# Kernel tuning notes

Hardware: AMD Instinct MI355X
Metric: run time of the kernel (lower is better)

Reference implementation:

```python
import jax, jax.numpy as jnp
import numpy as np

B, T_Q, T_K, D = 16, 512, 1024, 512


def setup_inputs() -> dict:
    key = jax.random.key(0)
    k1, k2, k3, k4, k5 = jax.random.split(key, 5)
    query = jax.random.normal(k1, (B, T_Q, D), dtype=jnp.float32)
    keys = jax.random.normal(k2, (B, T_K, D), dtype=jnp.float32)
    # lengths in [T_K//2, T_K] so every query row has valid keys
    output_lengths = jax.random.randint(k3, (B,), T_K // 2, T_K + 1, dtype=jnp.int32)
    # linear_q params (PyTorch Linear: y = x @ W.T + b), kaiming-ish scale
    Wq = jax.random.normal(k4, (D, D), dtype=jnp.float32) * (1.0 / np.sqrt(D))
    bq = jax.random.normal(k5, (D,), dtype=jnp.float32) * 0.01
    scale = jnp.ones((1,), dtype=jnp.float32)
    return {"query": query, "keys": keys, "output_lengths": output_lengths,
            "Wq": Wq, "bq": bq, "scale": scale}


def reference(query, keys, output_lengths, Wq, bq, scale):
    # linear_q: b t_q d -> b t_q d
    att_query = jnp.einsum('bqe,de->bqd', query, Wq) + bq
    # dot_prod score with learned scalar scale: b t_q t_k
    scores = jnp.einsum('bqd,bkd->bqk', att_query, keys) * scale[0]
    # length mask over t_k (True = valid position)
    valid = jnp.arange(keys.shape[1]) < output_lengths[:, None]  # b t_k
    neg_inf = jnp.asarray(-jnp.inf, dtype=scores.dtype)
    scores = jnp.where(valid[:, None, :], scores, neg_inf)
    attn = jax.nn.softmax(scores, axis=2)  # dropout p=0 -> identity
    # context = attn @ values, values == keys
    context = jnp.einsum('bqk,bkd->bqd', attn, keys)
    return context, attn
```

## Files before the change

### kernel.cpp

```cpp
#include <hip/hip_runtime.h>
#include <math.h>

#define BB 16
#define TQ 512
#define TK 1024
#define DD 512

typedef __bf16 bf16x8 __attribute__((ext_vector_type(8)));
typedef __bf16 bf16x4v __attribute__((ext_vector_type(4)));
typedef _Float16 f16x8 __attribute__((ext_vector_type(8)));
typedef _Float16 f16x4v __attribute__((ext_vector_type(4)));
typedef float f32x4 __attribute__((ext_vector_type(4)));

template<int TM, bool SPLIT, bool BT, bool BIAS, bool SCALE>
__global__ __launch_bounds__(256) void mfma_gemm(
    const float* __restrict__ A, const float* __restrict__ Bm,
    float* __restrict__ C, const float* __restrict__ bias,
    const float* __restrict__ scl,
    int N, int K, long sA, long sB, long sC)
{
    constexpr int WI  = TM / 32;
    constexpr int LDT = 40;
    __shared__ unsigned short As_hi[TM * LDT];
    __shared__ unsigned short Bs_hi[128 * LDT];
    __shared__ unsigned short As_lo[SPLIT ? TM * LDT : 8];
    __shared__ unsigned short Bs_lo[SPLIT ? 128 * LDT : 8];

    const int bz = blockIdx.z;
    A  += (long)bz * sA;
    Bm += (long)bz * sB;
    C  += (long)bz * sC;

    const int m0 = blockIdx.y * TM;
    const int n0 = blockIdx.x * 128;
    const int tid  = threadIdx.x;
    const int lane = tid & 63;
    const int wave = tid >> 6;
    const int wm0 = (wave >> 1) * (TM / 2);
    const int wn0 = (wave & 1) * 64;
    const int fm = lane & 15;
    const int fq = lane >> 4;

    f32x4 acc[WI][4];
    #pragma unroll
    for (int i = 0; i < WI; ++i)
        #pragma unroll
        for (int j = 0; j < 4; ++j) {
            f32x4 z = {0.f, 0.f, 0.f, 0.f};
            acc[i][j] = z;
        }

    for (int k0 = 0; k0 < K; k0 += 32) {
        #pragma unroll
        for (int i = 0; i < WI; ++i) {
            const int s   = tid + i * 256;
            const int row = s >> 3;
            const int c4  = (s & 7) << 2;
            const float4 v = *(const float4*)(A + (long)(m0 + row) * K + k0 + c4);
            if (SPLIT) {
                const __bf16 h0 = (__bf16)v.x, h1 = (__bf16)v.y,
                             h2 = (__bf16)v.z, h3 = (__bf16)v.w;
                bf16x4v hv = {h0, h1, h2, h3};
                *(bf16x4v*)&As_hi[row * LDT + c4] = hv;
                bf16x4v lv = {(__bf16)(v.x - (float)h0), (__bf16)(v.y - (float)h1),
                              (__bf16)(v.z - (float)h2), (__bf16)(v.w - (float)h3)};
                *(bf16x4v*)&As_lo[row * LDT + c4] = lv;
            } else {
                f16x4v hv = {(_Float16)v.x, (_Float16)v.y, (_Float16)v.z, (_Float16)v.w};
                *(f16x4v*)&As_hi[row * LDT + c4] = hv;
            }
        }
        if (BT) {
            #pragma unroll
            for (int i = 0; i < 4; ++i) {
                const int s   = tid + i * 256;
                const int row = s >> 3;
                const int c4  = (s & 7) << 2;
                const float4 v = *(const float4*)(Bm + (long)(n0 + row) * K + k0 + c4);
                if (SPLIT) {
                    const __bf16 h0 = (__bf16)v.x, h1 = (__bf16)v.y,
                                 h2 = (__bf16)v.z, h3 = (__bf16)v.w;
                    bf16x4v hv = {h0, h1, h2, h3};
                    *(bf16x4v*)&Bs_hi[row * LDT + c4] = hv;
                    bf16x4v lv = {(__bf16)(v.x - (float)h0), (__bf16)(v.y - (float)h1),
                                  (__bf16)(v.z - (float)h2), (__bf16)(v.w - (float)h3)};
                    *(bf16x4v*)&Bs_lo[row * LDT + c4] = lv;
                } else {
                    f16x4v hv = {(_Float16)v.x, (_Float16)v.y, (_Float16)v.z, (_Float16)v.w};
                    *(f16x4v*)&Bs_hi[row * LDT + c4] = hv;
                }
            }
        } else {
            const int n  = tid & 127;
            const int kh = tid >> 7;
            const float* src = Bm + (long)(k0 + kh * 16) * N + n0 + n;
            float xs[16];
            #pragma unroll
            for (int j2 = 0; j2 < 16; ++j2) xs[j2] = src[(long)j2 * N];
            #pragma unroll
            for (int w2 = 0; w2 < 4; ++w2) {
                if (SPLIT) {
                    const __bf16 h0 = (__bf16)xs[w2*4+0], h1 = (__bf16)xs[w2*4+1],
                                 h2 = (__bf16)xs[w2*4+2], h3 = (__bf16)xs[w2*4+3];
                    bf16x4v hv = {h0, h1, h2, h3};
                    *(bf16x4v*)&Bs_hi[n * LDT + kh * 16 + w2 * 4] = hv;
                    bf16x4v lv = {(__bf16)(xs[w2*4+0] - (float)h0),
                                  (__bf16)(xs[w2*4+1] - (float)h1),
                                  (__bf16)(xs[w2*4+2] - (float)h2),
                                  (__bf16)(xs[w2*4+3] - (float)h3)};
                    *(bf16x4v*)&Bs_lo[n * LDT + kh * 16 + w2 * 4] = lv;
                } else {
                    f16x4v hv = {(_Float16)xs[w2*4+0], (_Float16)xs[w2*4+1],
                                 (_Float16)xs[w2*4+2], (_Float16)xs[w2*4+3]};
                    *(f16x4v*)&Bs_hi[n * LDT + kh * 16 + w2 * 4] = hv;
                }
            }
        }
        __syncthreads();

        if (SPLIT) {
            bf16x8 ah[WI], al[WI], bh[4], bl[4];
            #pragma unroll
            for (int i = 0; i < WI; ++i) {
                const int ra = (wm0 + 16 * i + fm) * LDT + fq * 8;
                ah[i] = *(const bf16x8*)&As_hi[ra];
                al[i] = *(const bf16x8*)&As_lo[ra];
            }
            #pragma unroll
            for (int j = 0; j < 4; ++j) {
                const int rb = (wn0 + 16 * j + fm) * LDT + fq * 8;
                bh[j] = *(const bf16x8*)&Bs_hi[rb];
                bl[j] = *(const bf16x8*)&Bs_lo[rb];
            }
            #pragma unroll
            for (int i = 0; i < WI; ++i)
                #pragma unroll
                for (int j = 0; j < 4; ++j) {
                    acc[i][j] = __builtin_amdgcn_mfma_f32_16x16x32_bf16(ah[i], bh[j], acc[i][j], 0, 0, 0);
                    acc[i][j] = __builtin_amdgcn_mfma_f32_16x16x32_bf16(ah[i], bl[j], acc[i][j], 0, 0, 0);
                    acc[i][j] = __builtin_amdgcn_mfma_f32_16x16x32_bf16(al[i], bh[j], acc[i][j], 0, 0, 0);
                }
        } else {
            f16x8 fa[WI], fb[4];
            #pragma unroll
            for (int i = 0; i < WI; ++i)
                fa[i] = *(const f16x8*)&As_hi[(wm0 + 16 * i + fm) * LDT + fq * 8];
            #pragma unroll
            for (int j = 0; j < 4; ++j)
                fb[j] = *(const f16x8*)&Bs_hi[(wn0 + 16 * j + fm) * LDT + fq * 8];
            #pragma unroll
            for (int i = 0; i < WI; ++i)
                #pragma unroll
                for (int j = 0; j < 4; ++j)
                    acc[i][j] = __builtin_amdgcn_mfma_f32_16x16x32_f16(fa[i], fb[j], acc[i][j], 0, 0, 0);
        }
        __syncthreads();
    }

    const float s = SCALE ? scl[0] : 1.0f;
    #pragma unroll
    for (int i = 0; i < WI; ++i) {
        #pragma unroll
        for (int j = 0; j < 4; ++j) {
            const int n = n0 + wn0 + 16 * j + fm;
            float bv = BIAS ? bias[n] : 0.0f;
            #pragma unroll
            for (int r = 0; r < 4; ++r) {
                const int m = m0 + wm0 + 16 * i + fq * 4 + r;
                float v = acc[i][j][r] + bv;
                if (SCALE) v *= s;
                C[(long)m * N + n] = v;
            }
        }
    }
}

__global__ __launch_bounds__(256) void softmax_kernel(
    float* __restrict__ attn, const int* __restrict__ lens)
{
    const int row = blockIdx.x;
    const int b   = row >> 9;
    const int len = lens[b];
    float* p = attn + (long)row * TK;

    const int tid  = threadIdx.x;
    const int lane = tid & 63;
    const int wave = tid >> 6;
    const int k0   = tid * 4;

    const float4 v = *(const float4*)(p + k0);
    float x[4] = {v.x, v.y, v.z, v.w};
    float mx = -INFINITY;
    #pragma unroll
    for (int i = 0; i < 4; ++i) {
        if (k0 + i < len) mx = fmaxf(mx, x[i]);
        else x[i] = -INFINITY;
    }
    #pragma unroll
    for (int off = 32; off; off >>= 1) mx = fmaxf(mx, __shfl_xor(mx, off, 64));

    __shared__ float red[8];
    if (lane == 0) red[wave] = mx;
    __syncthreads();
    mx = fmaxf(fmaxf(red[0], red[1]), fmaxf(red[2], red[3]));

    float e[4];
    float sum = 0.0f;
    #pragma unroll
    for (int i = 0; i < 4; ++i) {
        e[i] = (x[i] > -INFINITY) ? __expf(x[i] - mx) : 0.0f;
        sum += e[i];
    }
    #pragma unroll
    for (int off = 32; off; off >>= 1) sum += __shfl_xor(sum, off, 64);
    if (lane == 0) red[4 + wave] = sum;
    __syncthreads();
    sum = red[4] + red[5] + red[6] + red[7];

    const float inv = 1.0f / sum;
    float4 o = {e[0] * inv, e[1] * inv, e[2] * inv, e[3] * inv};
    *(float4*)(p + k0) = o;
}

extern "C" void kernel_launch(void* const* d_in, const int* in_sizes, int n_in,
                              void* d_out, int out_size, void* d_ws, size_t ws_size,
                              hipStream_t stream) {
    (void)in_sizes; (void)n_in; (void)out_size; (void)d_ws; (void)ws_size;

    const float* query = (const float*)d_in[0];
    const float* keys  = (const float*)d_in[1];
    const int*   lens  = (const int*)d_in[2];
    const float* Wq    = (const float*)d_in[3];
    const float* bq    = (const float*)d_in[4];
    const float* scale = (const float*)d_in[5];

    float* out  = (float*)d_out;
    float* ctx  = out;
    float* attn = out + (size_t)BB * TQ * DD;
    float* aq   = ctx;

    mfma_gemm<64, false, true, true, false>
        <<<dim3(DD / 128, (BB * TQ) / 64, 1), 256, 0, stream>>>(
        query, Wq, aq, bq, nullptr, DD, DD, 0, 0, 0);

    mfma_gemm<128, true, true, false, true>
        <<<dim3(TK / 128, TQ / 128, BB), 256, 0, stream>>>(
        aq, keys, attn, nullptr, scale, TK, DD,
        (long)TQ * DD, (long)TK * DD, (long)TQ * TK);

    softmax_kernel<<<BB * TQ, 256, 0, stream>>>(attn, lens);

    mfma_gemm<64, false, false, false, false>
        <<<dim3(DD / 128, TQ / 64, BB), 256, 0, stream>>>(
        attn, keys, ctx, nullptr, nullptr, DD, TK,
        (long)TQ * TK, (long)TK * DD, (long)TQ * DD);
}
```

Before: 197.9 us.

## Pre-convert operands to 16-bit buffers and use direct global-to-LDS GEMM loads

Adds conversion kernels that write fp16 copies of query and Wq, and split bf16 hi/lo plus a transposed fp16 copy of keys, into workspace. A new GEMM kernel streams these 16-bit operands with global_load_lds into an XOR-swizzled LDS tile using K-step 64 and the 16x16x32 MFMA. The projection GEMM now emits hi/lo bf16 directly, and softmax also writes an fp16 attention copy for the context GEMM. The aim is to halve operand bytes and drop per-tile conversion work and strided loads, at the cost of extra conversion passes and workspace traffic. If the workspace is too small it falls back to the old path.

```diff
diff --git a/kernel.cpp b/kernel.cpp
--- a/kernel.cpp
+++ b/kernel.cpp
@@ -11,6 +11,208 @@
 typedef _Float16 f16x8 __attribute__((ext_vector_type(8)));
 typedef _Float16 f16x4v __attribute__((ext_vector_type(4)));
 typedef float f32x4 __attribute__((ext_vector_type(4)));
+
+__device__ __forceinline__ unsigned short f16b(float x) {
+    _Float16 h = (_Float16)x;
+    return __builtin_bit_cast(unsigned short, h);
+}
+__device__ __forceinline__ unsigned short bf16b(float x) {
+    __bf16 h = (__bf16)x;
+    return __builtin_bit_cast(unsigned short, h);
+}
+
+__device__ __forceinline__ void gload16(const void* g, void* l) {
+    __builtin_amdgcn_global_load_lds(
+        (const __attribute__((address_space(1))) unsigned int*)g,
+        (__attribute__((address_space(3))) unsigned int*)l, 16, 0, 0);
+}
+
+template<int TM, bool SPLIT, int OM, bool BIAS, bool SCALE>
+__global__ __launch_bounds__(256) void gemm16(
+    const unsigned short* __restrict__ A0, const unsigned short* __restrict__ A1,
+    const unsigned short* __restrict__ B0, const unsigned short* __restrict__ B1,
+    float* __restrict__ C, unsigned short* __restrict__ D0,
+    unsigned short* __restrict__ D1,
+    const float* __restrict__ bias, const float* __restrict__ scl,
+    int N, int K, long sA, long sB, long sC)
+{
+    constexpr int WI = TM / 32;
+    constexpr int IA = TM / 32;
+    __shared__ unsigned short As0[TM * 64];
+    __shared__ unsigned short Bs0[128 * 64];
+    __shared__ unsigned short As1[SPLIT ? TM * 64 : 8];
+    __shared__ unsigned short Bs1[SPLIT ? 128 * 64 : 8];
+
+    const int bz = blockIdx.z;
+    const long oA = (long)bz * sA, oB = (long)bz * sB;
+    const int m0 = blockIdx.y * TM;
+    const int n0 = blockIdx.x * 128;
+    const int tid = threadIdx.x, lane = tid & 63, wave = tid >> 6;
+    const int wm0 = (wave >> 1) * (TM / 2);
+    const int wn0 = (wave & 1) * 64;
+    const int fm = lane & 15, fq = lane >> 4;
+
+    f32x4 acc[WI][4];
+    #pragma unroll
+    for (int i = 0; i < WI; ++i)
+        #pragma unroll
+        for (int j = 0; j < 4; ++j) {
+            f32x4 z = {0.f, 0.f, 0.f, 0.f};
+            acc[i][j] = z;
+        }
+
+    for (int k0 = 0; k0 < K; k0 += 64) {
+        #pragma unroll
+        for (int t = 0; t < IA; ++t) {
+            const int sb = (wave * IA + t) * 64;
+            const int slot = sb + lane;
+            const int row = slot >> 3;
+            const int g = (slot & 7) ^ (row & 7);
+            const long ge = oA + (long)(m0 + row) * K + k0 + g * 8;
+            gload16(A0 + ge, &As0[sb * 8]);
+            if (SPLIT) gload16(A1 + ge, &As1[sb * 8]);
+        }
+        #pragma unroll
+        for (int t = 0; t < 4; ++t) {
+            const int sb = (wave * 4 + t) * 64;
+            const int slot = sb + lane;
+            const int row = slot >> 3;
+            const int g = (slot & 7) ^ (row & 7);
+            const long ge = oB + (long)(n0 + row) * K + k0 + g * 8;
+            gload16(B0 + ge, &Bs0[sb * 8]);
+            if (SPLIT) gload16(B1 + ge, &Bs1[sb * 8]);
+        }
+        __syncthreads();
+
+        #pragma unroll
+        for (int s = 0; s < 2; ++s) {
+            if (SPLIT) {
+                bf16x8 ah[WI], al[WI], bh[4], bl[4];
+                #pragma unroll
+                for (int i = 0; i < WI; ++i) {
+                    const int row = wm0 + 16 * i + fm;
+                    const int slot = row * 8 + ((s * 4 + fq) ^ (row & 7));
+                    ah[i] = *(const bf16x8*)&As0[slot * 8];
+                    al[i] = *(const bf16x8*)&As1[slot * 8];
+                }
+                #pragma unroll
+                for (int j = 0; j < 4; ++j) {
+                    const int row = wn0 + 16 * j + fm;
+                    const int slot = row * 8 + ((s * 4 + fq) ^ (row & 7));
+                    bh[j] = *(const bf16x8*)&Bs0[slot * 8];
+                    bl[j] = *(const bf16x8*)&Bs1[slot * 8];
+                }
+                #pragma unroll
+                for (int i = 0; i < WI; ++i)
+                    #pragma unroll
+                    for (int j = 0; j < 4; ++j) {
+                        acc[i][j] = __builtin_amdgcn_mfma_f32_16x16x32_bf16(ah[i], bh[j], acc[i][j], 0, 0, 0);
+                        acc[i][j] = __builtin_amdgcn_mfma_f32_16x16x32_bf16(ah[i], bl[j], acc[i][j], 0, 0, 0);
+                        acc[i][j] = __builtin_amdgcn_mfma_f32_16x16x32_bf16(al[i], bh[j], acc[i][j], 0, 0, 0);
+                    }
+            } else {
+                f16x8 fa[WI], fb[4];
+                #pragma unroll
+                for (int i = 0; i < WI; ++i) {
+                    const int row = wm0 + 16 * i + fm;
+                    const int slot = row * 8 + ((s * 4 + fq) ^ (row & 7));
+                    fa[i] = *(const f16x8*)&As0[slot * 8];
+                }
+                #pragma unroll
+                for (int j = 0; j < 4; ++j) {
+                    const int row = wn0 + 16 * j + fm;
+                    const int slot = row * 8 + ((s * 4 + fq) ^ (row & 7));
+                    fb[j] = *(const f16x8*)&Bs0[slot * 8];
+                }
+                #pragma unroll
+                for (int i = 0; i < WI; ++i)
+                    #pragma unroll
+                    for (int j = 0; j < 4; ++j)
+                        acc[i][j] = __builtin_amdgcn_mfma_f32_16x16x32_f16(fa[i], fb[j], acc[i][j], 0, 0, 0);
+            }
+        }
+        __syncthreads();
+    }
+
+    const float sv = SCALE ? scl[0] : 1.0f;
+    #pragma unroll
+    for (int i = 0; i < WI; ++i) {
+        #pragma unroll
+        for (int j = 0; j < 4; ++j) {
+            const int n = n0 + wn0 + 16 * j + fm;
+            const float bv = BIAS ? bias[n] : 0.0f;
+            #pragma unroll
+            for (int r = 0; r < 4; ++r) {
+                const int m = m0 + wm0 + 16 * i + fq * 4 + r;
+                float v = acc[i][j][r] + bv;
+                if (SCALE) v *= sv;
+                const long o = (long)bz * sC + (long)m * N + n;
+                if (OM == 0) {
+                    C[o] = v;
+                } else {
+                    const __bf16 h = (__bf16)v;
+                    D0[o] = __builtin_bit_cast(unsigned short, h);
+                    D1[o] = bf16b(v - (float)h);
+                }
+            }
+        }
+    }
+}
+
+__global__ __launch_bounds__(256) void cvt_qw_kernel(
+    const float* __restrict__ q, const float* __restrict__ w,
+    unsigned short* __restrict__ q16, unsigned short* __restrict__ w16,
+    int nq4, int nw4)
+{
+    const int t = blockIdx.x * 256 + threadIdx.x;
+    const float* s;
+    unsigned short* d;
+    if (t < nq4)            { s = q + (long)t * 4;         d = q16 + (long)t * 4; }
+    else if (t < nq4 + nw4) { s = w + (long)(t - nq4) * 4; d = w16 + (long)(t - nq4) * 4; }
+    else return;
+    const float4 v = *(const float4*)s;
+    f16x4v o = {(_Float16)v.x, (_Float16)v.y, (_Float16)v.z, (_Float16)v.w};
+    *(f16x4v*)d = o;
+}
+
+__global__ __launch_bounds__(256) void cvt_keys_kernel(
+    const float* __restrict__ keys, unsigned short* __restrict__ kh,
+    unsigned short* __restrict__ kl, unsigned short* __restrict__ kT)
+{
+    __shared__ unsigned short T[64][72];
+    const int b = blockIdx.z, kt = blockIdx.x, dt = blockIdx.y;
+    const int tid = threadIdx.x;
+    const float* src = keys + ((long)b * TK + (long)kt * 64) * DD + dt * 64;
+
+    #pragma unroll
+    for (int i = 0; i < 4; ++i) {
+        const int slot = tid + i * 256;
+        const int r  = slot >> 4;
+        const int c4 = (slot & 15) * 4;
+        const float4 v = *(const float4*)(src + (long)r * DD + c4);
+        const __bf16 h0 = (__bf16)v.x, h1 = (__bf16)v.y,
+                     h2 = (__bf16)v.z, h3 = (__bf16)v.w;
+        const long o = ((long)b * TK + kt * 64 + r) * DD + dt * 64 + c4;
+        bf16x4v hv = {h0, h1, h2, h3};
+        *(bf16x4v*)&kh[o] = hv;
+        bf16x4v lv = {(__bf16)(v.x - (float)h0), (__bf16)(v.y - (float)h1),
+                      (__bf16)(v.z - (float)h2), (__bf16)(v.w - (float)h3)};
+        *(bf16x4v*)&kl[o] = lv;
+        T[c4 + 0][r] = f16b(v.x);
+        T[c4 + 1][r] = f16b(v.y);
+        T[c4 + 2][r] = f16b(v.z);
+        T[c4 + 3][r] = f16b(v.w);
+    }
+    __syncthreads();
+    #pragma unroll
+    for (int i = 0; i < 4; ++i) {
+        const int slot = tid + i * 256;
+        const int c  = slot >> 4;
+        const int r4 = (slot & 15) * 4;
+        const ushort4 o4 = *(const ushort4*)&T[c][r4];
+        *(ushort4*)&kT[((long)b * DD + dt * 64 + c) * TK + kt * 64 + r4] = o4;
+    }
+}
 
 template<int TM, bool SPLIT, bool BT, bool BIAS, bool SCALE>
 __global__ __launch_bounds__(256) void mfma_gemm(
@@ -92,8 +294,8 @@
             }
         } else {
             const int n  = tid & 127;
-            const int kh = tid >> 7;
-            const float* src = Bm + (long)(k0 + kh * 16) * N + n0 + n;
+            const int kh2 = tid >> 7;
+            const float* src = Bm + (long)(k0 + kh2 * 16) * N + n0 + n;
             float xs[16];
             #pragma unroll
             for (int j2 = 0; j2 < 16; ++j2) xs[j2] = src[(long)j2 * N];
@@ -103,16 +305,16 @@
                     const __bf16 h0 = (__bf16)xs[w2*4+0], h1 = (__bf16)xs[w2*4+1],
                                  h2 = (__bf16)xs[w2*4+2], h3 = (__bf16)xs[w2*4+3];
                     bf16x4v hv = {h0, h1, h2, h3};
-                    *(bf16x4v*)&Bs_hi[n * LDT + kh * 16 + w2 * 4] = hv;
+                    *(bf16x4v*)&Bs_hi[n * LDT + kh2 * 16 + w2 * 4] = hv;
                     bf16x4v lv = {(__bf16)(xs[w2*4+0] - (float)h0),
                                   (__bf16)(xs[w2*4+1] - (float)h1),
                                   (__bf16)(xs[w2*4+2] - (float)h2),
                                   (__bf16)(xs[w2*4+3] - (float)h3)};
-                    *(bf16x4v*)&Bs_lo[n * LDT + kh * 16 + w2 * 4] = lv;
+                    *(bf16x4v*)&Bs_lo[n * LDT + kh2 * 16 + w2 * 4] = lv;
                 } else {
                     f16x4v hv = {(_Float16)xs[w2*4+0], (_Float16)xs[w2*4+1],
                                  (_Float16)xs[w2*4+2], (_Float16)xs[w2*4+3]};
-                    *(f16x4v*)&Bs_hi[n * LDT + kh * 16 + w2 * 4] = hv;
+                    *(f16x4v*)&Bs_hi[n * LDT + kh2 * 16 + w2 * 4] = hv;
                 }
             }
         }
@@ -176,7 +378,8 @@
 }
 
 __global__ __launch_bounds__(256) void softmax_kernel(
-    float* __restrict__ attn, const int* __restrict__ lens)
+    float* __restrict__ attn, unsigned short* __restrict__ attn16,
+    const int* __restrict__ lens)
 {
     const int row = blockIdx.x;
     const int b   = row >> 9;
@@ -218,14 +421,19 @@
     sum = red[4] + red[5] + red[6] + red[7];
 
     const float inv = 1.0f / sum;
-    float4 o = {e[0] * inv, e[1] * inv, e[2] * inv, e[3] * inv};
+    const float o0 = e[0] * inv, o1 = e[1] * inv, o2 = e[2] * inv, o3 = e[3] * inv;
+    float4 o = {o0, o1, o2, o3};
     *(float4*)(p + k0) = o;
+    if (attn16) {
+        f16x4v o16 = {(_Float16)o0, (_Float16)o1, (_Float16)o2, (_Float16)o3};
+        *(f16x4v*)&attn16[(long)row * TK + k0] = o16;
+    }
 }
 
 extern "C" void kernel_launch(void* const* d_in, const int* in_sizes, int n_in,
                               void* d_out, int out_size, void* d_ws, size_t ws_size,
                               hipStream_t stream) {
-    (void)in_sizes; (void)n_in; (void)out_size; (void)d_ws; (void)ws_size;
+    (void)in_sizes; (void)n_in; (void)out_size;
 
     const float* query = (const float*)d_in[0];
     const float* keys  = (const float*)d_in[1];
@@ -237,21 +445,59 @@
     float* out  = (float*)d_out;
     float* ctx  = out;
     float* attn = out + (size_t)BB * TQ * DD;
-    float* aq   = ctx;
-
-    mfma_gemm<64, false, true, true, false>
-        <<<dim3(DD / 128, (BB * TQ) / 64, 1), 256, 0, stream>>>(
-        query, Wq, aq, bq, nullptr, DD, DD, 0, 0, 0);
-
-    mfma_gemm<128, true, true, false, true>
-        <<<dim3(TK / 128, TQ / 128, BB), 256, 0, stream>>>(
-        aq, keys, attn, nullptr, scale, TK, DD,
-        (long)TQ * DD, (long)TK * DD, (long)TQ * TK);
-
-    softmax_kernel<<<BB * TQ, 256, 0, stream>>>(attn, lens);
-
-    mfma_gemm<64, false, false, false, false>
-        <<<dim3(DD / 128, TQ / 64, BB), 256, 0, stream>>>(
-        attn, keys, ctx, nullptr, nullptr, DD, TK,
-        (long)TQ * TK, (long)TK * DD, (long)TQ * DD);
-}
+
+    const size_t NQ  = (size_t)BB * TQ * DD;
+    const size_t NW  = (size_t)DD * DD;
+    const size_t NK  = (size_t)BB * TK * DD;
+    const size_t NAT = (size_t)BB * TQ * TK;
+    const size_t REQ = (NQ + NW + 2 * NQ + 3 * NK + NAT) * 2;
+
+    if (ws_size >= REQ) {
+        unsigned short* w = (unsigned short*)d_ws;
+        unsigned short* q16  = w;               w += NQ;
+        unsigned short* w16  = w;               w += NW;
+        unsigned short* aqh  = w;               w += NQ;
+        unsigned short* aql  = w;               w += NQ;
+        unsigned short* kh   = w;               w += NK;
+        unsigned short* kl   = w;               w += NK;
+        unsigned short* kT   = w;               w += NK;
+        unsigned short* at16 = w;
+
+        const int nq4 = (int)(NQ / 4), nw4 = (int)(NW / 4);
+        cvt_qw_kernel<<<(nq4 + nw4 + 255) / 256, 256, 0, stream>>>(
+            query, Wq, q16, w16, nq4, nw4);
+        cvt_keys_kernel<<<dim3(TK / 64, DD / 64, BB), 256, 0, stream>>>(
+            keys, kh, kl, kT);
+
+        gemm16<64, false, 1, true, false>
+            <<<dim3(DD / 128, (BB * TQ) / 64, 1), 256, 0, stream>>>(
+            q16, nullptr, w16, nullptr, nullptr, aqh, aql, bq, nullptr,
+            DD, DD, 0, 0, 0);
+
+        gemm16<128, true, 0, false, true>
+            <<<dim3(TK / 128, TQ / 128, BB), 256, 0, stream>>>(
+            aqh, aql, kh, kl, attn, nullptr, nullptr, nullptr, scale,
+            TK, DD, (long)TQ * DD, (long)TK * DD, (long)TQ * TK);
+
+        softmax_kernel<<<BB * TQ, 256, 0, stream>>>(attn, at16, lens);
+
+        gemm16<64, false, 0, false, false>
+            <<<dim3(DD / 128, TQ / 64, BB), 256, 0, stream>>>(
+            at16, nullptr, kT, nullptr, ctx, nullptr, nullptr, nullptr, nullptr,
+            DD, TK, (long)TQ * TK, (long)DD * TK, (long)TQ * DD);
+    } else {
+        float* aq = ctx;
+        mfma_gemm<64, false, true, true, false>
+            <<<dim3(DD / 128, (BB * TQ) / 64, 1), 256, 0, stream>>>(
+            query, Wq, aq, bq, nullptr, DD, DD, 0, 0, 0);
+        mfma_gemm<128, true, true, false, true>
+            <<<dim3(TK / 128, TQ / 128, BB), 256, 0, stream>>>(
+            aq, keys, attn, nullptr, scale, TK, DD,
+            (long)TQ * DD, (long)TK * DD, (long)TQ * TK);
+        softmax_kernel<<<BB * TQ, 256, 0, stream>>>(attn, nullptr, lens);
+        mfma_gemm<64, false, false, false, false>
+            <<<dim3(DD / 128, TQ / 64, BB), 256, 0, stream>>>(
+            attn, keys, ctx, nullptr, nullptr, DD, TK,
+            (long)TQ * TK, (long)TK * DD, (long)TQ * DD);
+    }
+}
```

Measured after the change: 189.5 us. -4.2%, faster.
